# Kernel tuning notes

Measured on AMD Instinct MI355X. Metric: run time of the kernel, lower is better.

The kernel has to match this reference:

```python
import jax, jax.numpy as jnp
import numpy as np


def setup_inputs() -> dict:
    key = jax.random.key(0)
    k1, k2 = jax.random.split(key)
    B, C, F, H, W = 2, 19, 4, 256, 384
    inp = jax.random.uniform(k1, (B, C, F, H, W), dtype=jnp.float32)
    target = jax.random.randint(k2, (B, F, H, W), 0, C, dtype=jnp.int64)
    return {"input": inp, "target": target}


def reference(input, target):
    """Multi-class Lovasz-Softmax loss, vectorized over classes.

    input:  [B, C, F, H, W] class probabilities in [0, 1]
    target: [B, F, H, W] integer labels in [0, C)
    (No ignore_index values present in the generated inputs, so the
    valid-pixel filter of the original is a no-op.)
    """
    B, C, F, H, W = input.shape
    # flatten to [N, C] pixels-by-classes, matching permute(0,2,3,4,1).view(-1,C)
    probs = jnp.transpose(input, (0, 2, 3, 4, 1)).reshape(-1, C)
    labels = target.reshape(-1)  # [N]

    fg = (labels[:, None] == jnp.arange(C)[None, :]).astype(probs.dtype)  # [N, C]
    errors = jnp.abs(fg - probs)  # [N, C]

    # descending sort per class column (one batched sort instead of C kernels)
    perm = jnp.argsort(-errors, axis=0)  # [N, C]
    errors_sorted = jnp.take_along_axis(errors, perm, axis=0)
    fg_sorted = jnp.take_along_axis(fg, perm, axis=0)

    # Lovasz gradient (Alg. 1), per class
    gts = jnp.sum(fg, axis=0)  # [C]
    intersection = gts[None, :] - jnp.cumsum(fg_sorted, axis=0)
    union = gts[None, :] + jnp.cumsum(1.0 - fg_sorted, axis=0)
    jaccard = 1.0 - intersection / union
    grad = jnp.concatenate([jaccard[:1], jaccard[1:] - jaccard[:-1]], axis=0)

    per_class_loss = jnp.sum(errors_sorted * grad, axis=0)  # [C]

    # mean over classes that are present (fg.sum() > 0), like the loop's `continue`
    present = gts > 0
    n_present = jnp.maximum(jnp.sum(present.astype(probs.dtype)), 1.0)
    return jnp.sum(jnp.where(present, per_class_loss, 0.0)) / n_present
```

## Files before the change

kernel.cpp:

```cpp
#include <hip/hip_runtime.h>
#include <hip/hip_bf16.h>


#define NCLS   19
#define FHW    393216
#define NPIX   786432
#define NB     2048
#define PIXPB  8192
#define NCHUNK (NPIX / PIXPB)
#define BPT    (NB / 256)

#define GH_WORDS (NCLS * NB)
#define LAB_OFF  (GH_WORDS * 4)
#define CL_OFF   (LAB_OFF + NPIX)

__device__ __forceinline__ void accum_one(unsigned int* h, float p, int lab, int c) {
    bool fg = (lab == c);
    float e = fg ? (1.0f - p) : p;
    unsigned int bits = __float_as_uint(1.0f + e);
    unsigned int bkt = (bits - 0x3F800000u) >> 12;
    bkt = min(bkt, (unsigned int)(NB - 1));
    atomicAdd(&h[bkt], 1u + (fg ? (1u << 20) : 0u));
}

__global__ __launch_bounds__(256) void prep_kernel(
        const int4* __restrict__ tgt4, uchar4* __restrict__ lab4,
        unsigned int* __restrict__ gH) {
    const int i = blockIdx.x * 256 + threadIdx.x;
    int4 l = tgt4[i];
    lab4[i] = make_uchar4((unsigned char)l.x, (unsigned char)l.y,
                          (unsigned char)l.z, (unsigned char)l.w);
    if (i < GH_WORDS) gH[i] = 0u;
}

__global__ __launch_bounds__(256) void hist_kernel(
        const float* __restrict__ input, const unsigned char* __restrict__ lab,
        unsigned int* __restrict__ gH) {
    __shared__ unsigned int h[NB];
    const int tid = threadIdx.x;
    const int c = blockIdx.y;
    const int chunk = blockIdx.x;

    #pragma unroll
    for (int i = tid; i < NB; i += 256) h[i] = 0u;
    __syncthreads();

    const int pix0 = chunk * PIXPB;
    const int b = pix0 / FHW;
    const int fhw0 = pix0 % FHW;
    const float4* __restrict__ p4 =
        (const float4*)(input + ((long long)(b * NCLS + c)) * FHW + fhw0);
    const uchar4* __restrict__ l4 = (const uchar4*)(lab + pix0);

    #pragma unroll
    for (int i = tid; i < PIXPB / 4; i += 256) {
        float4 p = p4[i];
        uchar4 l = l4[i];
        accum_one(h, p.x, l.x, c);
        accum_one(h, p.y, l.y, c);
        accum_one(h, p.z, l.z, c);
        accum_one(h, p.w, l.w, c);
    }
    __syncthreads();

    unsigned int* __restrict__ g = gH + c * NB;
    #pragma unroll
    for (int i = tid; i < NB; i += 256) {
        unsigned int v = h[i];
        if (v) atomicAdd(&g[i], v);
    }
}

__global__ __launch_bounds__(256) void scan_kernel(
        const unsigned int* __restrict__ gH,
        float* __restrict__ classLoss, unsigned int* __restrict__ Gtot) {
    const int c = blockIdx.x;
    const int tid = threadIdx.x;
    const unsigned int* __restrict__ g = gH + c * NB;

    unsigned int w[BPT];
    const int base = NB - BPT * (tid + 1);
    unsigned int sumN = 0, sumG = 0;
    #pragma unroll
    for (int j = 0; j < BPT; ++j) {
        w[j] = g[base + j];
        sumN += w[j] & 0xFFFFFu;
        sumG += w[j] >> 20;
    }

    __shared__ unsigned long long sd[256];
    const unsigned long long mine = ((unsigned long long)sumG << 32) | sumN;
    sd[tid] = mine;
    __syncthreads();
    for (int off = 1; off < 256; off <<= 1) {
        unsigned long long add = (tid >= off) ? sd[tid - off] : 0ull;
        __syncthreads();
        sd[tid] += add;
        __syncthreads();
    }
    const unsigned long long incl = sd[tid];
    const unsigned long long tot = sd[255];
    const unsigned long long exc = incl - mine;
    const unsigned int G = (unsigned int)(tot >> 32);

    if (G == 0) { if (tid == 0) { classLoss[c] = 0.0f; Gtot[c] = 0u; } return; }

    const float Gf = (float)G;
    unsigned int r = (unsigned int)exc;
    unsigned int cf = (unsigned int)(exc >> 32);
    float acc = 0.0f;
    #pragma unroll
    for (int j = BPT - 1; j >= 0; --j) {
        const unsigned int nb = w[j] & 0xFFFFFu;
        const unsigned int gb = w[j] >> 20;
        if (nb) {
            const float r0 = (float)r,          c0 = (float)cf;
            const float r1 = (float)(r + nb),   c1 = (float)(cf + gb);
            const float J0 = 1.0f - (Gf - c0) / (Gf + r0 - c0);
            const float J1 = 1.0f - (Gf - c1) / (Gf + r1 - c1);
            const float center = ((float)(base + j) + 0.5f) * (1.0f / (float)NB);
            acc += center * (J1 - J0);
        }
        r += nb; cf += gb;
    }

    __shared__ float sf[256];
    sf[tid] = acc;
    __syncthreads();
    for (int off = 128; off > 0; off >>= 1) {
        if (tid < off) sf[tid] += sf[tid + off];
        __syncthreads();
    }
    if (tid == 0) { classLoss[c] = sf[0]; Gtot[c] = G; }
}

__global__ void finalize_kernel(const unsigned int* __restrict__ Gtot,
                                const float* __restrict__ classLoss,
                                float* __restrict__ out) {
    if (threadIdx.x == 0 && blockIdx.x == 0) {
        float s = 0.0f; int cnt = 0;
        for (int c = 0; c < NCLS; ++c) {
            if (Gtot[c] > 0u) { s += classLoss[c]; ++cnt; }
        }
        out[0] = s / fmaxf((float)cnt, 1.0f);
    }
}

extern "C" void kernel_launch(void* const* d_in, const int* in_sizes, int n_in,
                              void* d_out, int out_size, void* d_ws, size_t ws_size,
                              hipStream_t stream) {
    const float* input = (const float*)d_in[0];
    const int* target = (const int*)d_in[1];
    float* out = (float*)d_out;

    unsigned int* gH = (unsigned int*)d_ws;
    unsigned char* lab = (unsigned char*)d_ws + LAB_OFF;
    float* classLoss = (float*)((unsigned char*)d_ws + CL_OFF);
    unsigned int* Gtot = (unsigned int*)(classLoss + NCLS);

    prep_kernel<<<NPIX / 4 / 256, 256, 0, stream>>>(
        (const int4*)target, (uchar4*)lab, gH);
    hist_kernel<<<dim3(NCHUNK, NCLS), 256, 0, stream>>>(input, lab, gH);
    scan_kernel<<<NCLS, 256, 0, stream>>>(gH, classLoss, Gtot);
    finalize_kernel<<<1, 64, 0, stream>>>(Gtot, classLoss, out);
}
```

Before: 104.1 us.

## Replace global histogram atomics with per-block scratch and separate reduction kernel

Each histogram block now writes its whole shared-memory histogram to a private slice of scratch memory with plain vector stores, in place of atomically adding the nonzero buckets into a global histogram. A new reduce kernel sums the 96 per-chunk histograms for each class and bucket, so the zeroing of the global histogram in the prep kernel is dropped. This removes global atomic contention but adds an extra kernel launch and about 15 MB of scratch traffic written and then read back.

```diff
diff --git a/kernel.cpp b/kernel.cpp
--- a/kernel.cpp
+++ b/kernel.cpp
@@ -10,9 +10,10 @@
 #define NCHUNK (NPIX / PIXPB)
 #define BPT    (NB / 256)
 
-#define GH_WORDS (NCLS * NB)
-#define LAB_OFF  (GH_WORDS * 4)
-#define CL_OFF   (LAB_OFF + NPIX)
+#define SCR_WORDS (NCHUNK * NCLS * NB)
+#define GHF_OFF   (SCR_WORDS * 4)
+#define LAB_OFF   (GHF_OFF + NCLS * NB * 4)
+#define CL_OFF    (LAB_OFF + NPIX)
 
 __device__ __forceinline__ void accum_one(unsigned int* h, float p, int lab, int c) {
     bool fg = (lab == c);
@@ -24,18 +25,16 @@
 }
 
 __global__ __launch_bounds__(256) void prep_kernel(
-        const int4* __restrict__ tgt4, uchar4* __restrict__ lab4,
-        unsigned int* __restrict__ gH) {
+        const int4* __restrict__ tgt4, uchar4* __restrict__ lab4) {
     const int i = blockIdx.x * 256 + threadIdx.x;
     int4 l = tgt4[i];
     lab4[i] = make_uchar4((unsigned char)l.x, (unsigned char)l.y,
                           (unsigned char)l.z, (unsigned char)l.w);
-    if (i < GH_WORDS) gH[i] = 0u;
 }
 
 __global__ __launch_bounds__(256) void hist_kernel(
         const float* __restrict__ input, const unsigned char* __restrict__ lab,
-        unsigned int* __restrict__ gH) {
+        unsigned int* __restrict__ scratch) {
     __shared__ unsigned int h[NB];
     const int tid = threadIdx.x;
     const int c = blockIdx.y;
@@ -63,12 +62,21 @@
     }
     __syncthreads();
 
-    unsigned int* __restrict__ g = gH + c * NB;
+    uint4* __restrict__ dst = (uint4*)(scratch + ((c * NCHUNK + chunk) * NB));
+    const uint4* __restrict__ src = (const uint4*)h;
     #pragma unroll
-    for (int i = tid; i < NB; i += 256) {
-        unsigned int v = h[i];
-        if (v) atomicAdd(&g[i], v);
-    }
+    for (int i = tid; i < NB / 4; i += 256) dst[i] = src[i];
+}
+
+__global__ __launch_bounds__(256) void reduce_kernel(
+        const unsigned int* __restrict__ scratch, unsigned int* __restrict__ gH) {
+    const int c = blockIdx.y;
+    const int bkt = blockIdx.x * 256 + threadIdx.x;
+    const unsigned int* __restrict__ src = scratch + (long long)c * NCHUNK * NB + bkt;
+    unsigned int s = 0;
+    #pragma unroll 8
+    for (int k = 0; k < NCHUNK; ++k) s += src[(long long)k * NB];
+    gH[c * NB + bkt] = s;
 }
 
 __global__ __launch_bounds__(256) void scan_kernel(
@@ -153,14 +161,15 @@
     const int* target = (const int*)d_in[1];
     float* out = (float*)d_out;
 
-    unsigned int* gH = (unsigned int*)d_ws;
+    unsigned int* scratch = (unsigned int*)d_ws;
+    unsigned int* gH = (unsigned int*)((unsigned char*)d_ws + GHF_OFF);
     unsigned char* lab = (unsigned char*)d_ws + LAB_OFF;
     float* classLoss = (float*)((unsigned char*)d_ws + CL_OFF);
     unsigned int* Gtot = (unsigned int*)(classLoss + NCLS);
 
-    prep_kernel<<<NPIX / 4 / 256, 256, 0, stream>>>(
-        (const int4*)target, (uchar4*)lab, gH);
-    hist_kernel<<<dim3(NCHUNK, NCLS), 256, 0, stream>>>(input, lab, gH);
+    prep_kernel<<<NPIX / 4 / 256, 256, 0, stream>>>((const int4*)target, (uchar4*)lab);
+    hist_kernel<<<dim3(NCHUNK, NCLS), 256, 0, stream>>>(input, lab, scratch);
+    reduce_kernel<<<dim3(NB / 256, NCLS), 256, 0, stream>>>(scratch, gH);
     scan_kernel<<<NCLS, 256, 0, stream>>>(gH, classLoss, Gtot);
     finalize_kernel<<<1, 64, 0, stream>>>(Gtot, classLoss, out);
 }
```

Result: no change. 105.7 us (+1.6%).

## Replicate global histograms, prefetch hist loads, fuse finalize into scan

Applied to the files above, without the earlier changes.

Global histograms are split into 8 copies so that the per-block atomic merges spread across more addresses and contend less. The scan sums the copies back together. The hist kernel now issues all of its global loads into registers before the shared-histogram atomics, which lets memory latency overlap the zeroing barrier. The finalize kernel is removed: the last scan block, found with an atomic done counter, computes the mean, saving one launch. The cost is more zeroing work in prep and eight times more reads in the scan.

```diff
diff --git a/kernel.cpp b/kernel.cpp
--- a/kernel.cpp
+++ b/kernel.cpp
@@ -9,10 +9,13 @@
 #define PIXPB  8192
 #define NCHUNK (NPIX / PIXPB)
 #define BPT    (NB / 256)
+#define NCOPY  8
 
-#define GH_WORDS (NCLS * NB)
-#define LAB_OFF  (GH_WORDS * 4)
-#define CL_OFF   (LAB_OFF + NPIX)
+#define GH_WORDS  (NCOPY * NCLS * NB)
+#define DONE_IDX  GH_WORDS
+#define CL_IDX    (GH_WORDS + 1)
+#define GT_IDX    (GH_WORDS + 20)
+#define LAB_OFF   1310720
 
 __device__ __forceinline__ void accum_one(unsigned int* h, float p, int lab, int c) {
     bool fg = (lab == c);
@@ -30,7 +33,9 @@
     int4 l = tgt4[i];
     lab4[i] = make_uchar4((unsigned char)l.x, (unsigned char)l.y,
                           (unsigned char)l.z, (unsigned char)l.w);
-    if (i < GH_WORDS) gH[i] = 0u;
+    gH[i] = 0u;
+    const int k = i + 196608;
+    if (k <= DONE_IDX) gH[k] = 0u;
 }
 
 __global__ __launch_bounds__(256) void hist_kernel(
@@ -43,7 +48,6 @@
 
     #pragma unroll
     for (int i = tid; i < NB; i += 256) h[i] = 0u;
-    __syncthreads();
 
     const int pix0 = chunk * PIXPB;
     const int b = pix0 / FHW;
@@ -52,18 +56,26 @@
         (const float4*)(input + ((long long)(b * NCLS + c)) * FHW + fhw0);
     const uchar4* __restrict__ l4 = (const uchar4*)(lab + pix0);
 
+    float4 pr[8];
+    uchar4 lr[8];
     #pragma unroll
-    for (int i = tid; i < PIXPB / 4; i += 256) {
-        float4 p = p4[i];
-        uchar4 l = l4[i];
-        accum_one(h, p.x, l.x, c);
-        accum_one(h, p.y, l.y, c);
-        accum_one(h, p.z, l.z, c);
-        accum_one(h, p.w, l.w, c);
+    for (int j = 0; j < 8; ++j) {
+        pr[j] = p4[tid + 256 * j];
+        lr[j] = l4[tid + 256 * j];
     }
     __syncthreads();
 
-    unsigned int* __restrict__ g = gH + c * NB;
+    #pragma unroll
+    for (int j = 0; j < 8; ++j) {
+        accum_one(h, pr[j].x, lr[j].x, c);
+        accum_one(h, pr[j].y, lr[j].y, c);
+        accum_one(h, pr[j].z, lr[j].z, c);
+        accum_one(h, pr[j].w, lr[j].w, c);
+    }
+    __syncthreads();
+
+    const int copy = (blockIdx.y * NCHUNK + blockIdx.x) & (NCOPY - 1);
+    unsigned int* __restrict__ g = gH + (copy * NCLS + c) * NB;
     #pragma unroll
     for (int i = tid; i < NB; i += 256) {
         unsigned int v = h[i];
@@ -72,21 +84,27 @@
 }
 
 __global__ __launch_bounds__(256) void scan_kernel(
-        const unsigned int* __restrict__ gH,
-        float* __restrict__ classLoss, unsigned int* __restrict__ Gtot) {
+        unsigned int* __restrict__ gH, float* __restrict__ out) {
     const int c = blockIdx.x;
     const int tid = threadIdx.x;
-    const unsigned int* __restrict__ g = gH + c * NB;
 
-    unsigned int w[BPT];
+    unsigned int nj[BPT], gj[BPT];
     const int base = NB - BPT * (tid + 1);
     unsigned int sumN = 0, sumG = 0;
     #pragma unroll
-    for (int j = 0; j < BPT; ++j) {
-        w[j] = g[base + j];
-        sumN += w[j] & 0xFFFFFu;
-        sumG += w[j] >> 20;
+    for (int j = 0; j < BPT; ++j) { nj[j] = 0u; gj[j] = 0u; }
+    #pragma unroll
+    for (int k = 0; k < NCOPY; ++k) {
+        const unsigned int* __restrict__ g = gH + (k * NCLS + c) * NB;
+        #pragma unroll
+        for (int j = 0; j < BPT; ++j) {
+            unsigned int v = g[base + j];
+            nj[j] += v & 0xFFFFFu;
+            gj[j] += v >> 20;
+        }
     }
+    #pragma unroll
+    for (int j = 0; j < BPT; ++j) { sumN += nj[j]; sumG += gj[j]; }
 
     __shared__ unsigned long long sd[256];
     const unsigned long long mine = ((unsigned long long)sumG << 32) | sumN;
@@ -103,46 +121,54 @@
     const unsigned long long exc = incl - mine;
     const unsigned int G = (unsigned int)(tot >> 32);
 
-    if (G == 0) { if (tid == 0) { classLoss[c] = 0.0f; Gtot[c] = 0u; } return; }
-
-    const float Gf = (float)G;
-    unsigned int r = (unsigned int)exc;
-    unsigned int cf = (unsigned int)(exc >> 32);
-    float acc = 0.0f;
-    #pragma unroll
-    for (int j = BPT - 1; j >= 0; --j) {
-        const unsigned int nb = w[j] & 0xFFFFFu;
-        const unsigned int gb = w[j] >> 20;
-        if (nb) {
-            const float r0 = (float)r,          c0 = (float)cf;
-            const float r1 = (float)(r + nb),   c1 = (float)(cf + gb);
-            const float J0 = 1.0f - (Gf - c0) / (Gf + r0 - c0);
-            const float J1 = 1.0f - (Gf - c1) / (Gf + r1 - c1);
-            const float center = ((float)(base + j) + 0.5f) * (1.0f / (float)NB);
-            acc += center * (J1 - J0);
+    float classAcc = 0.0f;
+    if (G > 0) {
+        const float Gf = (float)G;
+        unsigned int r = (unsigned int)exc;
+        unsigned int cf = (unsigned int)(exc >> 32);
+        float acc = 0.0f;
+        #pragma unroll
+        for (int j = BPT - 1; j >= 0; --j) {
+            const unsigned int nb = nj[j];
+            const unsigned int gb = gj[j];
+            if (nb) {
+                const float r0 = (float)r,        c0 = (float)cf;
+                const float r1 = (float)(r + nb), c1 = (float)(cf + gb);
+                const float J0 = 1.0f - (Gf - c0) / (Gf + r0 - c0);
+                const float J1 = 1.0f - (Gf - c1) / (Gf + r1 - c1);
+                const float center = ((float)(base + j) + 0.5f) * (1.0f / (float)NB);
+                acc += center * (J1 - J0);
+            }
+            r += nb; cf += gb;
         }
-        r += nb; cf += gb;
+        __shared__ float sf[256];
+        sf[tid] = acc;
+        __syncthreads();
+        for (int off = 128; off > 0; off >>= 1) {
+            if (tid < off) sf[tid] += sf[tid + off];
+            __syncthreads();
+        }
+        classAcc = sf[0];
     }
 
-    __shared__ float sf[256];
-    sf[tid] = acc;
-    __syncthreads();
-    for (int off = 128; off > 0; off >>= 1) {
-        if (tid < off) sf[tid] += sf[tid + off];
-        __syncthreads();
-    }
-    if (tid == 0) { classLoss[c] = sf[0]; Gtot[c] = G; }
-}
-
-__global__ void finalize_kernel(const unsigned int* __restrict__ Gtot,
-                                const float* __restrict__ classLoss,
-                                float* __restrict__ out) {
-    if (threadIdx.x == 0 && blockIdx.x == 0) {
-        float s = 0.0f; int cnt = 0;
-        for (int c = 0; c < NCLS; ++c) {
-            if (Gtot[c] > 0u) { s += classLoss[c]; ++cnt; }
+    if (tid == 0) {
+        float* classLoss = (float*)(gH + CL_IDX);
+        unsigned int* Gtot = gH + GT_IDX;
+        unsigned int* done = gH + DONE_IDX;
+        classLoss[c] = classAcc;
+        Gtot[c] = G;
+        __threadfence();
+        unsigned int old = atomicAdd(done, 1u);
+        if (old == NCLS - 1) {
+            __threadfence();
+            const volatile float* vcl = (const volatile float*)classLoss;
+            const volatile unsigned int* vgt = (const volatile unsigned int*)Gtot;
+            float s = 0.0f; int cnt = 0;
+            for (int cc = 0; cc < NCLS; ++cc) {
+                if (vgt[cc] > 0u) { s += vcl[cc]; ++cnt; }
+            }
+            out[0] = s / fmaxf((float)cnt, 1.0f);
         }
-        out[0] = s / fmaxf((float)cnt, 1.0f);
     }
 }
 
@@ -155,12 +181,9 @@
 
     unsigned int* gH = (unsigned int*)d_ws;
     unsigned char* lab = (unsigned char*)d_ws + LAB_OFF;
-    float* classLoss = (float*)((unsigned char*)d_ws + CL_OFF);
-    unsigned int* Gtot = (unsigned int*)(classLoss + NCLS);
 
     prep_kernel<<<NPIX / 4 / 256, 256, 0, stream>>>(
         (const int4*)target, (uchar4*)lab, gH);
     hist_kernel<<<dim3(NCHUNK, NCLS), 256, 0, stream>>>(input, lab, gH);
-    scan_kernel<<<NCLS, 256, 0, stream>>>(gH, classLoss, Gtot);
-    finalize_kernel<<<1, 64, 0, stream>>>(Gtot, classLoss, out);
+    scan_kernel<<<NCLS, 256, 0, stream>>>(gH, out);
 }
```

New measurement: 105.0 us (median of 2 runs). Within noise of the previous version (+0.9%).
